# Kernel optimization log

Measured on AMD Instinct MI355X. Metric: run time of the kernel, lower is better.

The kernel has to match this reference:

```python
import jax, jax.numpy as jnp
import numpy as np
from jax import lax

B, T = 8192, 4096


def setup_inputs() -> dict:
    key = jax.random.key(0)
    kx, k1, k2, k3, k4 = jax.random.split(key, 5)
    # torch.nn.RNN default init: U(-1/sqrt(hidden), 1/sqrt(hidden)) = U(-1, 1) for hidden=1
    u = lambda k, shp: jax.random.uniform(k, shp, jnp.float32, -1.0, 1.0)
    return {
        "x": jax.random.normal(kx, (B, T, 1), jnp.float32),
        "w_ih": u(k1, (1, 1)),
        "w_hh": u(k2, (1, 1)),
        "b_ih": u(k3, (1,)),
        "b_hh": u(k4, (1,)),
    }


def reference(x, w_ih, w_hh, b_ih, b_hh):
    # Vanilla tanh RNN: h_t = tanh(x_t @ W_ih^T + b_ih + h_{t-1} @ W_hh^T + b_hh)
    # hidden=input=1, so all matmuls are scalar multiplies. Output is h at last step.
    a = w_ih[0, 0]
    b = w_hh[0, 0]
    c = b_ih[0] + b_hh[0]
    xT = jnp.swapaxes(x, 0, 1)  # [T, B, 1]

    def step(h, x_t):
        h_new = jnp.tanh(x_t * a + h * b + c)
        return h_new, None

    h0 = jnp.zeros((x.shape[0], 1), x.dtype)
    hT, _ = lax.scan(step, h0, xT)
    return hT  # [B, 1], equals rnn_output[:, -1]
```

## Files before the change

kernel.cpp:

```cpp
#include <hip/hip_runtime.h>


constexpr int T_LEN = 4096;
constexpr int LCH   = 64;
constexpr int NF4   = LCH / 4;

#define STEP_PG(qv)                                                     \
    do {                                                                \
        float r_ = __builtin_amdgcn_rcpf(E + 1.0f);                     \
        P *= (fourb * r_) * (1.0f - r_);                                \
        E = __builtin_amdgcn_exp2f(fmaf(r_, nB4, (qv)));                \
    } while (0)

__global__ __launch_bounds__(64)
void rnn_row_kernel(const float* __restrict__ x,
                    const float* __restrict__ w_ih,
                    const float* __restrict__ w_hh,
                    const float* __restrict__ b_ih,
                    const float* __restrict__ b_hh,
                    float* __restrict__ out) {
    __shared__ float4 sm[T_LEN / 4];
    const int lane = threadIdx.x;
    const int row  = blockIdx.x;

    const float a  = w_ih[0];
    const float bb = w_hh[0];
    const float cc = b_ih[0] + b_hh[0];

    const float L2E2  = 2.88539008177792681472f;
    const float A2    = a * L2E2;
    const float C2    = (bb + cc) * L2E2;
    const float nB4   = -(bb * L2E2 * 2.0f);
    const float fourb = 4.0f * bb;

    const float4* xp = (const float4*)(x + (size_t)row * T_LEN);
#pragma unroll
    for (int p = 0; p < 16; ++p) {
        int s = p * 64 + lane;
        sm[s ^ ((s >> 4) & 7)] = xp[s];
    }
    __syncthreads();

    float4 buf[NF4];
#pragma unroll
    for (int q = 0; q < NF4; ++q) {
        int s = lane * NF4 + q;
        buf[q] = sm[s ^ ((s >> 4) & 7)];
    }

    float E, P = 1.0f;
    {
        float4 v = buf[0];
        float q0 = fmaf(v.x, A2, C2);
        float q1 = fmaf(v.y, A2, C2);
        float q2 = fmaf(v.z, A2, C2);
        float q3 = fmaf(v.w, A2, C2);
        E = __builtin_amdgcn_exp2f(fmaf(0.5f, nB4, q0));
        STEP_PG(q1); STEP_PG(q2); STEP_PG(q3);
    }
#pragma unroll
    for (int i = 1; i < NF4; ++i) {
        float4 v = buf[i];
        float q0 = fmaf(v.x, A2, C2);
        float q1 = fmaf(v.y, A2, C2);
        float q2 = fmaf(v.z, A2, C2);
        float q3 = fmaf(v.w, A2, C2);
        STEP_PG(q0); STEP_PG(q1); STEP_PG(q2); STEP_PG(q3);
    }

    float r = __builtin_amdgcn_rcpf(E + 1.0f);
    float G = fmaf(-2.0f, r, 1.0f);
    P *= (fourb * r) * (1.0f - r);

#pragma unroll
    for (int d = 1; d < 64; d <<= 1) {
        float Pl = __shfl_up(P, d, 64);
        float Gl = __shfl_up(G, d, 64);
        if (lane >= d) {
            G = fmaf(P, Gl, G);
            P *= Pl;
        }
    }

    if (lane == 63) out[row] = G;
}

extern "C" void kernel_launch(void* const* d_in, const int* in_sizes, int n_in,
                              void* d_out, int out_size, void* d_ws, size_t ws_size,
                              hipStream_t stream) {
    const float* x    = (const float*)d_in[0];
    const float* w_ih = (const float*)d_in[1];
    const float* w_hh = (const float*)d_in[2];
    const float* b_ih = (const float*)d_in[3];
    const float* b_hh = (const float*)d_in[4];
    float* out = (float*)d_out;

    const int B = out_size;
    dim3 grid(B), block(64);
    rnn_row_kernel<<<grid, block, 0, stream>>>(x, w_ih, w_hh, b_ih, b_hh, out);
}
```

Measured before the change: 193.2 us.

## Split each row across four wavefronts with shorter per-thread chunks and cross-wave combine

Each block now uses 256 threads instead of 64, so every thread handles a 16-element chunk rather than a 64-element one. This shortens the serial exp/rcp dependency chain per thread. The four per-wave scan results are merged through shared memory with a second barrier. Global loads switch to nontemporal hints and the LDS swizzle is adjusted to the new stride. The cost is more threads, more linearization error terms composed, and extra synchronization per row.

New measurement: 183.6 us. -5.0%, faster.

```diff
diff --git a/kernel.cpp b/kernel.cpp
--- a/kernel.cpp
+++ b/kernel.cpp
@@ -2,8 +2,13 @@
 
 
 constexpr int T_LEN = 4096;
-constexpr int LCH   = 64;
-constexpr int NF4   = LCH / 4;
+constexpr int NTHR  = 256;
+constexpr int CH    = T_LEN / NTHR;
+constexpr int NF4   = CH / 4;
+
+typedef float fx4 __attribute__((ext_vector_type(4)));
+
+__device__ __forceinline__ int swz(int s) { return s ^ ((s >> 2) & 7); }
 
 #define STEP_PG(qv)                                                     \
     do {                                                                \
@@ -12,15 +17,19 @@
         E = __builtin_amdgcn_exp2f(fmaf(r_, nB4, (qv)));                \
     } while (0)
 
-__global__ __launch_bounds__(64)
+__global__ __launch_bounds__(NTHR)
 void rnn_row_kernel(const float* __restrict__ x,
                     const float* __restrict__ w_ih,
                     const float* __restrict__ w_hh,
                     const float* __restrict__ b_ih,
                     const float* __restrict__ b_hh,
                     float* __restrict__ out) {
-    __shared__ float4 sm[T_LEN / 4];
-    const int lane = threadIdx.x;
+    __shared__ fx4 sm[T_LEN / 4];
+    __shared__ float wP[4], wG[4];
+
+    const int tid  = threadIdx.x;
+    const int lane = tid & 63;
+    const int wv   = tid >> 6;
     const int row  = blockIdx.x;
 
     const float a  = w_ih[0];
@@ -33,24 +42,21 @@
     const float nB4   = -(bb * L2E2 * 2.0f);
     const float fourb = 4.0f * bb;
 
-    const float4* xp = (const float4*)(x + (size_t)row * T_LEN);
+    const fx4* xp = (const fx4*)(x + (size_t)row * T_LEN);
 #pragma unroll
-    for (int p = 0; p < 16; ++p) {
-        int s = p * 64 + lane;
-        sm[s ^ ((s >> 4) & 7)] = xp[s];
+    for (int i = 0; i < 4; ++i) {
+        int s = i * NTHR + tid;
+        sm[swz(s)] = __builtin_nontemporal_load(&xp[s]);
     }
     __syncthreads();
 
-    float4 buf[NF4];
+    fx4 buf[NF4];
 #pragma unroll
-    for (int q = 0; q < NF4; ++q) {
-        int s = lane * NF4 + q;
-        buf[q] = sm[s ^ ((s >> 4) & 7)];
-    }
+    for (int q = 0; q < NF4; ++q) buf[q] = sm[swz(tid * NF4 + q)];
 
     float E, P = 1.0f;
     {
-        float4 v = buf[0];
+        fx4 v = buf[0];
         float q0 = fmaf(v.x, A2, C2);
         float q1 = fmaf(v.y, A2, C2);
         float q2 = fmaf(v.z, A2, C2);
@@ -60,14 +66,13 @@
     }
 #pragma unroll
     for (int i = 1; i < NF4; ++i) {
-        float4 v = buf[i];
+        fx4 v = buf[i];
         float q0 = fmaf(v.x, A2, C2);
         float q1 = fmaf(v.y, A2, C2);
         float q2 = fmaf(v.z, A2, C2);
         float q3 = fmaf(v.w, A2, C2);
         STEP_PG(q0); STEP_PG(q1); STEP_PG(q2); STEP_PG(q3);
     }
-
     float r = __builtin_amdgcn_rcpf(E + 1.0f);
     float G = fmaf(-2.0f, r, 1.0f);
     P *= (fourb * r) * (1.0f - r);
@@ -81,8 +86,16 @@
             P *= Pl;
         }
     }
+    if (lane == 63) { wP[wv] = P; wG[wv] = G; }
+    __syncthreads();
 
-    if (lane == 63) out[row] = G;
+    if (tid == 0) {
+        float h = wG[0];
+        h = fmaf(wP[1], h, wG[1]);
+        h = fmaf(wP[2], h, wG[2]);
+        h = fmaf(wP[3], h, wG[3]);
+        out[row] = h;
+    }
 }
 
 extern "C" void kernel_launch(void* const* d_in, const int* in_sizes, int n_in,
@@ -96,6 +109,6 @@
     float* out = (float*)d_out;
 
     const int B = out_size;
-    dim3 grid(B), block(64);
+    dim3 grid(B), block(NTHR);
     rnn_row_kernel<<<grid, block, 0, stream>>>(x, w_ih, w_hh, b_ih, b_hh, out);
 }
```
